# Optimization experiments

Measured on AMD Instinct MI355X. Metric: run time of the kernel, lower is better.

Reference implementation:

```python
import jax, jax.numpy as jnp
import numpy as np

B, T, D, H = 4, 2048, 1024, 16
HD = D // H  # head_dim = 64


def setup_inputs() -> dict:
    key = jax.random.key(0)
    ks = jax.random.split(key, 7)
    x = jax.random.normal(ks[0], (B, T, D), dtype=jnp.float32)
    engagement = jax.random.uniform(ks[1], (B, T), dtype=jnp.float32)
    mask = jax.random.uniform(ks[2], (B, T)) < 0.1  # True = masked-out key
    s = 1.0 / np.sqrt(D)
    qkv_w = jax.random.normal(ks[3], (3 * D, D), dtype=jnp.float32) * s
    qkv_b = jax.random.normal(ks[4], (3 * D,), dtype=jnp.float32) * 0.02
    out_w = jax.random.normal(ks[5], (D, D), dtype=jnp.float32) * s
    out_b = jax.random.normal(ks[6], (D,), dtype=jnp.float32) * 0.02
    return {"x": x, "engagement": engagement, "mask": mask,
            "qkv_w": qkv_w, "qkv_b": qkv_b, "out_w": out_w, "out_b": out_b}


def reference(x, engagement, mask, qkv_w, qkv_b, out_w, out_b):
    b, t, d = x.shape
    qkv = x @ qkv_w.T + qkv_b                       # [B,T,3D]
    q, k, v = jnp.split(qkv, 3, axis=-1)
    # [B,T,D] -> [B,H,T,HD]
    to_heads = lambda a: a.reshape(b, t, H, HD).transpose(0, 2, 1, 3)
    q, k, v = to_heads(q), to_heads(k), to_heads(v)
    attn = jnp.einsum('bhqd,bhkd->bhqk', q, k) / jnp.sqrt(jnp.float32(HD))
    log_g = jnp.log(jnp.clip(engagement, 1e-6))     # [B,T] per-key bias
    attn = attn + log_g[:, None, None, :]
    attn = jnp.where(mask[:, None, None, :], jnp.float32(-1e9), attn)
    p = jax.nn.softmax(attn, axis=-1)
    o = jnp.einsum('bhqk,bhkd->bhqd', p, v)         # [B,H,T,HD]
    o = o.transpose(0, 2, 1, 3).reshape(b, t, d)    # [B,T,D]
    return o @ out_w.T + out_b
```

## Files before the change

kernel.cpp:

```cpp
#include <hip/hip_runtime.h>
#include <math.h>

#define B_  4
#define T_  2048
#define D_  1024
#define H_  16
#define HD_ 64

typedef unsigned short ushort_t;
typedef unsigned int uint_t;
typedef __attribute__((ext_vector_type(8))) short bf16x8;
typedef __attribute__((ext_vector_type(4))) float f32x4;

#define SC_LOG2 0.1803368801111243f

__device__ inline ushort_t f2bf(float f) {
  uint_t u = __float_as_uint(f);
  u += 0x7fffu + ((u >> 16) & 1u);
  return (ushort_t)(u >> 16);
}
__device__ inline ushort_t f2bf_fast(float f) {
  return (ushort_t)((__float_as_uint(f) + 0x8000u) >> 16);
}
__device__ inline uint_t pack2bf(float a, float b) {
  uint_t ua = (__float_as_uint(a) + 0x8000u) >> 16;
  uint_t ub = (__float_as_uint(b) + 0x8000u) & 0xffff0000u;
  return ua | ub;
}

__device__ inline void gload_lds16(const ushort_t* g, ushort_t* l) {
  __builtin_amdgcn_global_load_lds(
      (const __attribute__((address_space(1))) unsigned int*)g,
      (__attribute__((address_space(3))) unsigned int*)l, 16, 0, 0);
}

__global__ __launch_bounds__(256) void cvt_bf16(const float* __restrict__ in,
                                                ushort_t* __restrict__ out, int n) {
  int i = (blockIdx.x * 256 + threadIdx.x) * 4;
  if (i + 3 < n) {
    float4 v = *(const float4*)(in + i);
    uint_t lo = (uint_t)f2bf(v.x) | ((uint_t)f2bf(v.y) << 16);
    uint_t hi = (uint_t)f2bf(v.z) | ((uint_t)f2bf(v.w) << 16);
    *(uint2*)(out + i) = make_uint2(lo, hi);
  }
}

__global__ __launch_bounds__(256) void bias_prep(const float* __restrict__ eng,
                                                 const int* __restrict__ mask,
                                                 float* __restrict__ biasA, int n) {
  int i = blockIdx.x * 256 + threadIdx.x;
  if (i < n) biasA[i] = mask[i] ? -1e30f : __log2f(fmaxf(eng[i], 1e-6f));
}

template <int WRITE_BF16>
__global__ __launch_bounds__(256) void gemm_bf16(
    const ushort_t* __restrict__ A, const ushort_t* __restrict__ Bm,
    const float* __restrict__ bias, void* __restrict__ Cout,
    int M, int N, int K) {
  __shared__ __align__(16) ushort_t Ls[8192];
  ushort_t* As = Ls;
  ushort_t* Bs = Ls + 4096;
  const int tid = threadIdx.x;
  const int w = tid >> 6, lane = tid & 63;
  const int l15 = lane & 15, quad = lane >> 4;
  const int wm = w >> 1, wn = w & 1;
  const int m0 = blockIdx.y * 128, n0 = blockIdx.x * 128;

  f32x4 acc[4][4];
#pragma unroll
  for (int a = 0; a < 4; ++a)
#pragma unroll
    for (int b = 0; b < 4; ++b) acc[a][b] = (f32x4){0.f, 0.f, 0.f, 0.f};

  const int sr = lane >> 2;
  const int gc = (lane & 3) ^ ((sr >> 1) & 3);

  for (int k0 = 0; k0 < K; k0 += 32) {
    __syncthreads();
#pragma unroll
    for (int u = 0; u < 2; ++u) {
      int row = w * 32 + u * 16 + sr;
      gload_lds16(A + (size_t)(m0 + row) * K + k0 + gc * 8,
                  &As[(w * 32 + u * 16) * 32]);
      gload_lds16(Bm + (size_t)(n0 + row) * K + k0 + gc * 8,
                  &Bs[(w * 32 + u * 16) * 32]);
    }
    __syncthreads();
    bf16x8 af[4], bf[4];
#pragma unroll
    for (int mb = 0; mb < 4; ++mb) {
      int row = wm * 64 + mb * 16 + l15;
      int p = quad ^ ((l15 >> 1) & 3);
      af[mb] = *(const bf16x8*)(&As[row * 32 + p * 8]);
    }
#pragma unroll
    for (int nb = 0; nb < 4; ++nb) {
      int row = wn * 64 + nb * 16 + l15;
      int p = quad ^ ((l15 >> 1) & 3);
      bf[nb] = *(const bf16x8*)(&Bs[row * 32 + p * 8]);
    }
#pragma unroll
    for (int mb = 0; mb < 4; ++mb)
#pragma unroll
      for (int nb = 0; nb < 4; ++nb)
        acc[mb][nb] = __builtin_amdgcn_mfma_f32_16x16x32_bf16(
            af[mb], bf[nb], acc[mb][nb], 0, 0, 0);
  }

  float bb[4];
#pragma unroll
  for (int nb = 0; nb < 4; ++nb) bb[nb] = bias[n0 + wn * 64 + nb * 16 + l15];

  if (WRITE_BF16) {
    ushort_t* Cb = (ushort_t*)Cout;
#pragma unroll
    for (int mb = 0; mb < 4; ++mb) {
      __syncthreads();
#pragma unroll
      for (int nb = 0; nb < 4; ++nb)
#pragma unroll
        for (int i = 0; i < 4; ++i) {
          float v = acc[mb][nb][i] + bb[nb];
          Ls[(wm * 16 + quad * 4 + i) * 136 + wn * 64 + nb * 16 + l15] =
              f2bf_fast(v);
        }
      __syncthreads();
      int lr = tid >> 3, c = tid & 7;
      size_t gr = (size_t)(m0 + (lr >> 4) * 64 + mb * 16 + (lr & 15));
      uint4 v0 = *(const uint4*)&Ls[lr * 136 + c * 16];
      uint4 v1 = *(const uint4*)&Ls[lr * 136 + c * 16 + 8];
      *(uint4*)&Cb[gr * N + n0 + c * 16] = v0;
      *(uint4*)&Cb[gr * N + n0 + c * 16 + 8] = v1;
    }
  } else {
    float* Cf = (float*)Cout;
#pragma unroll
    for (int mb = 0; mb < 4; ++mb)
#pragma unroll
      for (int i = 0; i < 4; ++i) {
        size_t row = (size_t)(m0 + wm * 64 + mb * 16 + quad * 4 + i);
#pragma unroll
        for (int nb = 0; nb < 4; ++nb)
          Cf[row * N + n0 + wn * 64 + nb * 16 + l15] = acc[mb][nb][i] + bb[nb];
      }
  }
}

__global__ __launch_bounds__(256) void attn_mfma(
    const ushort_t* __restrict__ qkv, const float* __restrict__ biasA,
    ushort_t* __restrict__ oat) {
  __shared__ __align__(16) ushort_t Kb[64 * 64];
  __shared__ __align__(16) ushort_t Vb[8 * 520];
  __shared__ __align__(16) float bsh[64];
  __shared__ __align__(16) float lsum[4][32];
  __shared__ __align__(16) ushort_t Ost[4][32 * 72];

  const int b = blockIdx.z, h = blockIdx.y;
  const int q0 = blockIdx.x * 128;
  const int tid = threadIdx.x;
  const int w = tid >> 6, lane = tid & 63;
  const int l15 = lane & 15, quad = lane >> 4;
  const size_t rs = 3 * D_;

  bf16x8 qf[2][2];
#pragma unroll
  for (int qb = 0; qb < 2; ++qb) {
    const ushort_t* qp =
        qkv + (size_t)(b * T_ + q0 + w * 32 + qb * 16 + l15) * rs + h * HD_;
    qf[qb][0] = *(const bf16x8*)(qp + quad * 8);
    qf[qb][1] = *(const bf16x8*)(qp + 32 + quad * 8);
  }

  f32x4 Oa[2][4];
#pragma unroll
  for (int qb = 0; qb < 2; ++qb)
#pragma unroll
    for (int nb = 0; nb < 4; ++nb) Oa[qb][nb] = (f32x4){0.f, 0.f, 0.f, 0.f};
  float rsum[2] = {0.f, 0.f};

  const ushort_t* kbase = qkv + (size_t)(b * T_) * rs + D_ + h * HD_;
  const ushort_t* vbase = kbase + D_;
  const float* bptr = biasA + b * T_;

  const int kr = lane >> 3, kc = lane & 7;
  const int kgc = kc ^ kr;

  for (int k0 = 0; k0 < T_; k0 += 64) {
    __syncthreads();
#pragma unroll
    for (int u = 0; u < 2; ++u) {
      int key = w * 16 + u * 8 + kr;
      gload_lds16(kbase + (size_t)(k0 + key) * rs + kgc * 8,
                  &Kb[(w * 16 + u * 8) * 64]);
    }
    {
      int kp = tid & 31, c = tid >> 5;
      const ushort_t* v0p = vbase + (size_t)(k0 + 2 * kp) * rs + c * 8;
      uint4 va = *(const uint4*)v0p;
      uint4 vc = *(const uint4*)(v0p + rs);
      int gp = (kp >> 4) * 4 + ((kp >> 1) & 3);
      int j0 = ((kp >> 3) & 1) * 4 + 2 * (kp & 1);
      uint_t* dst = (uint_t*)&Vb[gp * 520 + c * 64 + j0];
      dst[0]  = (va.x & 0xffffu) | (vc.x << 16);
      dst[4]  = (va.x >> 16)     | (vc.x & 0xffff0000u);
      dst[8]  = (va.y & 0xffffu) | (vc.y << 16);
      dst[12] = (va.y >> 16)     | (vc.y & 0xffff0000u);
      dst[16] = (va.z & 0xffffu) | (vc.z << 16);
      dst[20] = (va.z >> 16)     | (vc.z & 0xffff0000u);
      dst[24] = (va.w & 0xffffu) | (vc.w << 16);
      dst[28] = (va.w >> 16)     | (vc.w & 0xffff0000u);
    }
    if (tid < 64) bsh[tid] = bptr[k0 + tid];
    __syncthreads();

    bf16x8 kf0[4], kf1[4];
#pragma unroll
    for (int nb = 0; nb < 4; ++nb) {
      int key = nb * 16 + l15;
      int p0 = (quad ^ (key & 7)) * 8;
      kf0[nb] = *(const bf16x8*)(&Kb[key * 64 + p0]);
      kf1[nb] = *(const bf16x8*)(&Kb[key * 64 + (p0 ^ 32)]);
    }
    bf16x8 vf0[4], vf1[4];
#pragma unroll
    for (int nbd = 0; nbd < 4; ++nbd) {
      vf0[nbd] = *(const bf16x8*)(&Vb[quad * 520 + (nbd * 16 + l15) * 8]);
      vf1[nbd] = *(const bf16x8*)(&Vb[(4 + quad) * 520 + (nbd * 16 + l15) * 8]);
    }

#pragma unroll
    for (int qb = 0; qb < 2; ++qb) {
      f32x4 st[4];
#pragma unroll
      for (int nb = 0; nb < 4; ++nb) {
        f32x4 s = (f32x4){0.f, 0.f, 0.f, 0.f};
        s = __builtin_amdgcn_mfma_f32_16x16x32_bf16(kf0[nb], qf[qb][0], s, 0, 0, 0);
        s = __builtin_amdgcn_mfma_f32_16x16x32_bf16(kf1[nb], qf[qb][1], s, 0, 0, 0);
        st[nb] = s;
      }
      float pp[4][4];
      float racc = 0.f;
#pragma unroll
      for (int nb = 0; nb < 4; ++nb) {
        f32x4 bv = *(const f32x4*)&bsh[nb * 16 + quad * 4];
#pragma unroll
        for (int i = 0; i < 4; ++i) {
          float p = __builtin_amdgcn_exp2f(st[nb][i] * SC_LOG2 + bv[i]);
          pp[nb][i] = p;
          racc += p;
        }
      }
      rsum[qb] += racc;
      union { uint4 u; bf16x8 v; } pf0, pf1;
      pf0.u.x = pack2bf(pp[0][0], pp[0][1]);
      pf0.u.y = pack2bf(pp[0][2], pp[0][3]);
      pf0.u.z = pack2bf(pp[1][0], pp[1][1]);
      pf0.u.w = pack2bf(pp[1][2], pp[1][3]);
      pf1.u.x = pack2bf(pp[2][0], pp[2][1]);
      pf1.u.y = pack2bf(pp[2][2], pp[2][3]);
      pf1.u.z = pack2bf(pp[3][0], pp[3][1]);
      pf1.u.w = pack2bf(pp[3][2], pp[3][3]);
#pragma unroll
      for (int nbd = 0; nbd < 4; ++nbd) {
        Oa[qb][nbd] = __builtin_amdgcn_mfma_f32_16x16x32_bf16(
            pf0.v, vf0[nbd], Oa[qb][nbd], 0, 0, 0);
        Oa[qb][nbd] = __builtin_amdgcn_mfma_f32_16x16x32_bf16(
            pf1.v, vf1[nbd], Oa[qb][nbd], 0, 0, 0);
      }
    }
  }

#pragma unroll
  for (int qb = 0; qb < 2; ++qb) {
    float r = rsum[qb];
    r += __shfl_xor(r, 16, 64);
    r += __shfl_xor(r, 32, 64);
    if (lane < 16) lsum[w][qb * 16 + lane] = r;
  }
#pragma unroll
  for (int qb = 0; qb < 2; ++qb) {
    f32x4 lr = *(const f32x4*)&lsum[w][qb * 16 + quad * 4];
    f32x4 invl;
#pragma unroll
    for (int i = 0; i < 4; ++i) invl[i] = 1.0f / lr[i];
#pragma unroll
    for (int nbd = 0; nbd < 4; ++nbd)
#pragma unroll
      for (int i = 0; i < 4; ++i)
        Ost[w][(qb * 16 + quad * 4 + i) * 72 + nbd * 16 + l15] =
            f2bf_fast(Oa[qb][nbd][i] * invl[i]);
  }
  ushort_t* dst = oat + (size_t)(b * T_ + q0 + w * 32) * D_ + h * HD_;
#pragma unroll
  for (int pp = 0; pp < 4; ++pp) {
    int row = pp * 8 + (lane >> 3), c = lane & 7;
    uint4 v = *(const uint4*)&Ost[w][row * 72 + c * 8];
    *(uint4*)&dst[(size_t)row * D_ + c * 8] = v;
  }
}

extern "C" void kernel_launch(void* const* d_in, const int* in_sizes, int n_in,
                              void* d_out, int out_size, void* d_ws, size_t ws_size,
                              hipStream_t stream) {
  const float* x     = (const float*)d_in[0];
  const float* eng   = (const float*)d_in[1];
  const int*   mask  = (const int*)d_in[2];
  const float* qkv_w = (const float*)d_in[3];
  const float* qkv_b = (const float*)d_in[4];
  const float* out_w = (const float*)d_in[5];
  const float* out_b = (const float*)d_in[6];
  float* out = (float*)d_out;

  const int M = B_ * T_;
  const size_t nx = (size_t)M * D_;
  const size_t nwq = (size_t)3 * D_ * D_;
  const size_t nwo = (size_t)D_ * D_;
  const size_t nqkv = (size_t)M * 3 * D_;

  char* p = (char*)d_ws;
  ushort_t* xb    = (ushort_t*)p;            p += nx * 2;
  ushort_t* wqkvb = (ushort_t*)p;            p += nwq * 2;
  ushort_t* woutb = (ushort_t*)p;            p += nwo * 2;
  ushort_t* qkvb  = (ushort_t*)p;            p += nqkv * 2;
  ushort_t* oatb  = (ushort_t*)p;            p += nx * 2;
  float*    biasA = (float*)p;               p += (size_t)M * 4;

  cvt_bf16<<<(int)(nx / 1024), 256, 0, stream>>>(x, xb, (int)nx);
  cvt_bf16<<<(int)(nwq / 1024), 256, 0, stream>>>(qkv_w, wqkvb, (int)nwq);
  cvt_bf16<<<(int)(nwo / 1024), 256, 0, stream>>>(out_w, woutb, (int)nwo);
  bias_prep<<<M / 256, 256, 0, stream>>>(eng, mask, biasA, M);

  gemm_bf16<1><<<dim3(3 * D_ / 128, M / 128), 256, 0, stream>>>(
      xb, wqkvb, qkv_b, qkvb, M, 3 * D_, D_);
  attn_mfma<<<dim3(T_ / 128, H_, B_), 256, 0, stream>>>(qkvb, biasA, oatb);
  gemm_bf16<0><<<dim3(D_ / 128, M / 128), 256, 0, stream>>>(
      oatb, woutb, out_b, out, M, D_, D_);
}
```

Measured before the change: 345.2 us.

## Double-buffer K/V tiles in attention kernel to overlap loads with MFMA

The attention kernel now keeps two LDS buffers for the K, V and bias tiles and prefetches the next tile (global-to-LDS K loads, V register loads) while computing on the current one. The V repack store happens after the compute, and there is one barrier per tile instead of two. Shared memory is combined into one aliased array, with the output staging reusing the K buffer region, and launch bounds now request 4 blocks per CU. The goal is to hide global load latency behind the MFMA work. The cost is more LDS per block and more live registers for the prefetched V data, which may limit occupancy.

```diff
diff --git a/kernel.cpp b/kernel.cpp
--- a/kernel.cpp
+++ b/kernel.cpp
@@ -32,6 +32,19 @@
   __builtin_amdgcn_global_load_lds(
       (const __attribute__((address_space(1))) unsigned int*)g,
       (__attribute__((address_space(3))) unsigned int*)l, 16, 0, 0);
+}
+
+__device__ inline void v_pack_store(ushort_t* Vb, uint4 va, uint4 vc,
+                                    int gp, int cc, int j0) {
+  uint_t* dst = (uint_t*)&Vb[gp * 520 + cc * 64 + j0];
+  dst[0]  = (va.x & 0xffffu) | (vc.x << 16);
+  dst[4]  = (va.x >> 16)     | (vc.x & 0xffff0000u);
+  dst[8]  = (va.y & 0xffffu) | (vc.y << 16);
+  dst[12] = (va.y >> 16)     | (vc.y & 0xffff0000u);
+  dst[16] = (va.z & 0xffffu) | (vc.z << 16);
+  dst[20] = (va.z >> 16)     | (vc.z & 0xffff0000u);
+  dst[24] = (va.w & 0xffffu) | (vc.w << 16);
+  dst[28] = (va.w >> 16)     | (vc.w & 0xffff0000u);
 }
 
 __global__ __launch_bounds__(256) void cvt_bf16(const float* __restrict__ in,
@@ -146,14 +159,17 @@
   }
 }
 
-__global__ __launch_bounds__(256) void attn_mfma(
+__global__ __launch_bounds__(256, 4) void attn_mfma(
     const ushort_t* __restrict__ qkv, const float* __restrict__ biasA,
     ushort_t* __restrict__ oat) {
-  __shared__ __align__(16) ushort_t Kb[64 * 64];
-  __shared__ __align__(16) ushort_t Vb[8 * 520];
-  __shared__ __align__(16) float bsh[64];
-  __shared__ __align__(16) float lsum[4][32];
-  __shared__ __align__(16) ushort_t Ost[4][32 * 72];
+  __shared__ __align__(16) char smem[34048];
+  ushort_t* Kb0 = (ushort_t*)(smem);
+  ushort_t* Kb1 = (ushort_t*)(smem + 8192);
+  ushort_t* Vb0 = (ushort_t*)(smem + 16384);
+  ushort_t* Vb1 = (ushort_t*)(smem + 24704);
+  float* bsh0 = (float*)(smem + 33024);
+  float* bsh1 = (float*)(smem + 33280);
+  float (*lsum)[32] = (float (*)[32])(smem + 33536);
 
   const int b = blockIdx.z, h = blockIdx.y;
   const int q0 = blockIdx.x * 128;
@@ -184,48 +200,52 @@
 
   const int kr = lane >> 3, kc = lane & 7;
   const int kgc = kc ^ kr;
-
-  for (int k0 = 0; k0 < T_; k0 += 64) {
-    __syncthreads();
-#pragma unroll
-    for (int u = 0; u < 2; ++u) {
-      int key = w * 16 + u * 8 + kr;
-      gload_lds16(kbase + (size_t)(k0 + key) * rs + kgc * 8,
-                  &Kb[(w * 16 + u * 8) * 64]);
-    }
-    {
-      int kp = tid & 31, c = tid >> 5;
-      const ushort_t* v0p = vbase + (size_t)(k0 + 2 * kp) * rs + c * 8;
-      uint4 va = *(const uint4*)v0p;
-      uint4 vc = *(const uint4*)(v0p + rs);
-      int gp = (kp >> 4) * 4 + ((kp >> 1) & 3);
-      int j0 = ((kp >> 3) & 1) * 4 + 2 * (kp & 1);
-      uint_t* dst = (uint_t*)&Vb[gp * 520 + c * 64 + j0];
-      dst[0]  = (va.x & 0xffffu) | (vc.x << 16);
-      dst[4]  = (va.x >> 16)     | (vc.x & 0xffff0000u);
-      dst[8]  = (va.y & 0xffffu) | (vc.y << 16);
-      dst[12] = (va.y >> 16)     | (vc.y & 0xffff0000u);
-      dst[16] = (va.z & 0xffffu) | (vc.z << 16);
-      dst[20] = (va.z >> 16)     | (vc.z & 0xffff0000u);
-      dst[24] = (va.w & 0xffffu) | (vc.w << 16);
-      dst[28] = (va.w >> 16)     | (vc.w & 0xffff0000u);
-    }
-    if (tid < 64) bsh[tid] = bptr[k0 + tid];
-    __syncthreads();
+  const int kp = tid & 31, cc = tid >> 5;
+  const int gp = (kp >> 4) * 4 + ((kp >> 1) & 3);
+  const int j0 = ((kp >> 3) & 1) * 4 + 2 * (kp & 1);
+
+  {
+#pragma unroll
+    for (int u = 0; u < 2; ++u)
+      gload_lds16(kbase + (size_t)(w * 16 + u * 8 + kr) * rs + kgc * 8,
+                  &Kb0[(w * 16 + u * 8) * 64]);
+    const ushort_t* vp = vbase + (size_t)(2 * kp) * rs + cc * 8;
+    uint4 va = *(const uint4*)vp;
+    uint4 vc = *(const uint4*)(vp + rs);
+    if (tid < 64) bsh0[tid] = bptr[tid];
+    v_pack_store(Vb0, va, vc, gp, cc, j0);
+  }
+  __syncthreads();
+
+  auto tile = [&](int k0, const ushort_t* Kc, const ushort_t* Vc,
+                  const float* bc, ushort_t* Kn, ushort_t* Vn, float* bn,
+                  bool pf) {
+    uint4 va, vc2;
+    if (pf) {
+      const int k1 = k0 + 64;
+#pragma unroll
+      for (int u = 0; u < 2; ++u)
+        gload_lds16(kbase + (size_t)(k1 + w * 16 + u * 8 + kr) * rs + kgc * 8,
+                    &Kn[(w * 16 + u * 8) * 64]);
+      const ushort_t* vp = vbase + (size_t)(k1 + 2 * kp) * rs + cc * 8;
+      va = *(const uint4*)vp;
+      vc2 = *(const uint4*)(vp + rs);
+      if (tid < 64) bn[tid] = bptr[k1 + tid];
+    }
 
     bf16x8 kf0[4], kf1[4];
 #pragma unroll
     for (int nb = 0; nb < 4; ++nb) {
       int key = nb * 16 + l15;
       int p0 = (quad ^ (key & 7)) * 8;
-      kf0[nb] = *(const bf16x8*)(&Kb[key * 64 + p0]);
-      kf1[nb] = *(const bf16x8*)(&Kb[key * 64 + (p0 ^ 32)]);
+      kf0[nb] = *(const bf16x8*)(&Kc[key * 64 + p0]);
+      kf1[nb] = *(const bf16x8*)(&Kc[key * 64 + (p0 ^ 32)]);
     }
     bf16x8 vf0[4], vf1[4];
 #pragma unroll
     for (int nbd = 0; nbd < 4; ++nbd) {
-      vf0[nbd] = *(const bf16x8*)(&Vb[quad * 520 + (nbd * 16 + l15) * 8]);
-      vf1[nbd] = *(const bf16x8*)(&Vb[(4 + quad) * 520 + (nbd * 16 + l15) * 8]);
+      vf0[nbd] = *(const bf16x8*)(&Vc[quad * 520 + (nbd * 16 + l15) * 8]);
+      vf1[nbd] = *(const bf16x8*)(&Vc[(4 + quad) * 520 + (nbd * 16 + l15) * 8]);
     }
 
 #pragma unroll
@@ -242,7 +262,7 @@
       float racc = 0.f;
 #pragma unroll
       for (int nb = 0; nb < 4; ++nb) {
-        f32x4 bv = *(const f32x4*)&bsh[nb * 16 + quad * 4];
+        f32x4 bv = *(const f32x4*)&bc[nb * 16 + quad * 4];
 #pragma unroll
         for (int i = 0; i < 4; ++i) {
           float p = __builtin_amdgcn_exp2f(st[nb][i] * SC_LOG2 + bv[i]);
@@ -268,6 +288,14 @@
             pf1.v, vf1[nbd], Oa[qb][nbd], 0, 0, 0);
       }
     }
+
+    if (pf) v_pack_store(Vn, va, vc2, gp, cc, j0);
+    __syncthreads();
+  };
+
+  for (int k0 = 0; k0 < T_; k0 += 128) {
+    tile(k0,      Kb0, Vb0, bsh0, Kb1, Vb1, bsh1, true);
+    tile(k0 + 64, Kb1, Vb1, bsh1, Kb0, Vb0, bsh0, k0 + 128 < T_);
   }
 
 #pragma unroll
@@ -277,6 +305,7 @@
     r += __shfl_xor(r, 32, 64);
     if (lane < 16) lsum[w][qb * 16 + lane] = r;
   }
+  ushort_t* OstW = (ushort_t*)(smem) + w * (32 * 72);
 #pragma unroll
   for (int qb = 0; qb < 2; ++qb) {
     f32x4 lr = *(const f32x4*)&lsum[w][qb * 16 + quad * 4];
@@ -287,14 +316,14 @@
     for (int nbd = 0; nbd < 4; ++nbd)
 #pragma unroll
       for (int i = 0; i < 4; ++i)
-        Ost[w][(qb * 16 + quad * 4 + i) * 72 + nbd * 16 + l15] =
+        OstW[(qb * 16 + quad * 4 + i) * 72 + nbd * 16 + l15] =
             f2bf_fast(Oa[qb][nbd][i] * invl[i]);
   }
   ushort_t* dst = oat + (size_t)(b * T_ + q0 + w * 32) * D_ + h * HD_;
 #pragma unroll
   for (int pp = 0; pp < 4; ++pp) {
     int row = pp * 8 + (lane >> 3), c = lane & 7;
-    uint4 v = *(const uint4*)&Ost[w][row * 72 + c * 8];
+    uint4 v = *(const uint4*)&OstW[row * 72 + c * 8];
     *(uint4*)&dst[(size_t)row * D_ + c * 8] = v;
   }
 }
```

Measured after the change: 1.003 ms. +190.7%, slower.
